# Performance work log

Measured on AMD Instinct MI355X. Metric: run time of the kernel, lower is better.

Reference implementation:

```python
import jax, jax.numpy as jnp
import numpy as np

LN_EPS = 1e-3  # keras LayerNormalization default
HEADS_GAT = 4

def _gelu(x):
    return jax.nn.gelu(x, approximate=False)  # keras 'gelu' is exact

def _ln(x, g, b):
    m = jnp.mean(x, axis=-1, keepdims=True)
    v = jnp.var(x, axis=-1, keepdims=True)
    return (x - m) / jnp.sqrt(v + LN_EPS) * g + b

def _gat(x, mask, w, a_src, a_dst, bias, heads):
    # dense-masked GAT: attention restricted to adj > 0.5 (self-loops present
    # since cosine-sim diagonal is 1). x: [BS, N, F]
    BS, N, _ = x.shape
    D = w.shape[1] // heads
    h = (x @ w).reshape(BS, N, heads, D)
    es = jnp.einsum('bnhd,hd->bnh', h, a_src)  # source term
    ed = jnp.einsum('bnhd,hd->bnh', h, a_dst)  # destination term
    # e[b,i,j,h]: edge j -> i
    e = jax.nn.leaky_relu(ed[:, :, None, :] + es[:, None, :, :], 0.2)
    e = jnp.where(mask[None, :, :, None], e, -1e9)
    alpha = jax.nn.softmax(e, axis=2)  # softmax over sources j
    out = jnp.einsum('bijh,bjhd->bihd', alpha, h).reshape(BS, N, heads * D)
    return out + bias

def _mha(x, wq, bq, wk, bk, wv, bv, wo, bo):
    q = jnp.einsum('bsf,fhd->bshd', x, wq) + bq
    k = jnp.einsum('bsf,fhd->bshd', x, wk) + bk
    v = jnp.einsum('bsf,fhd->bshd', x, wv) + bv
    s = jnp.einsum('bshd,bthd->bhst', q, k) / jnp.sqrt(jnp.asarray(q.shape[-1], x.dtype))
    a = jax.nn.softmax(s, axis=-1)
    o = jnp.einsum('bhst,bthd->bshd', a, v)
    return jnp.einsum('bshd,hdf->bsf', o, wo) + bo

def setup_inputs() -> dict:
    key = jax.random.key(0)
    ks = jax.random.split(key, 40)
    B, S, N = 4, 16, 400
    HID, OUT, DM, MH, DK, FF = 16, 32, 32, 2, 16, 64
    f32 = jnp.float32
    def glorot(k, shape, fin, fout):
        return jax.random.normal(k, shape, f32) * np.sqrt(2.0 / (fin + fout)).astype(np.float32)
    return {
        'x': jax.random.normal(ks[0], (B, S, N, 3), f32),
        'adj_embed': glorot(ks[1], (N, HID), N, HID),
        'proj_w': glorot(ks[2], (3, HID), 3, HID), 'proj_b': jnp.zeros((HID,), f32),
        'g1_w': glorot(ks[3], (HID, HID), HID, HID),
        'g1_asrc': glorot(ks[4], (4, HID // 4), HID, 4), 'g1_adst': glorot(ks[5], (4, HID // 4), HID, 4),
        'g1_b': jnp.zeros((HID,), f32),
        'g2_w': glorot(ks[6], (HID, OUT), HID, OUT),
        'g2_asrc': glorot(ks[7], (4, OUT // 4), OUT, 4), 'g2_adst': glorot(ks[8], (4, OUT // 4), OUT, 4),
        'g2_b': jnp.zeros((OUT,), f32),
        'wq': glorot(ks[9], (DM, MH, DK), DM, DM), 'bq': jnp.zeros((MH, DK), f32),
        'wk': glorot(ks[10], (DM, MH, DK), DM, DM), 'bk': jnp.zeros((MH, DK), f32),
        'wv': glorot(ks[11], (DM, MH, DK), DM, DM), 'bv': jnp.zeros((MH, DK), f32),
        'wo': glorot(ks[12], (MH, DK, DM), DM, DM), 'bo': jnp.zeros((DM,), f32),
        'ln1_g': jnp.ones((DM,), f32), 'ln1_b': jnp.zeros((DM,), f32),
        'f_w1': glorot(ks[13], (DM, FF), DM, FF), 'f_b1': jnp.zeros((FF,), f32),
        'f_w2': glorot(ks[14], (FF, DM), FF, DM), 'f_b2': jnp.zeros((DM,), f32),
        'ln2_g': jnp.ones((DM,), f32), 'ln2_b': jnp.zeros((DM,), f32),
        'r_w1': glorot(ks[15], (DM, 16), DM, 16), 'r_b1': jnp.zeros((16,), f32),
        'r_w2': glorot(ks[16], (16, 1), 16, 1), 'r_b2': jnp.zeros((1,), f32),
    }

def reference(x, adj_embed, proj_w, proj_b, g1_w, g1_asrc, g1_adst, g1_b,
              g2_w, g2_asrc, g2_adst, g2_b, wq, bq, wk, bk, wv, bv, wo, bo,
              ln1_g, ln1_b, f_w1, f_b1, f_w2, f_b2, ln2_g, ln2_b,
              r_w1, r_b1, r_w2, r_b2):
    B, S, N, _ = x.shape
    DM = 32
    xs = x.reshape(B * S, N, 3)
    # adaptive adjacency: cosine similarity of learned node embeddings
    emb = adj_embed / jnp.sqrt(jnp.maximum(jnp.sum(adj_embed * adj_embed, -1, keepdims=True), 1e-12))
    mask = (emb @ emb.T) > 0.5  # [N, N], shared across batch
    h = xs @ proj_w + proj_b
    h = _gelu(_gat(h, mask, g1_w, g1_asrc, g1_adst, g1_b, HEADS_GAT))
    h = _gat(h, mask, g2_w, g2_asrc, g2_adst, g2_b, HEADS_GAT)  # [B*S, N, 32]
    # faithful to source: plain reshape (no transpose) into temporal batch
    t = h.reshape(B, S, N, DM).reshape(B * N, S, DM)
    attn = _mha(t, wq, bq, wk, bk, wv, bv, wo, bo)
    t = _ln(t + attn, ln1_g, ln1_b)
    f = _gelu(t @ f_w1 + f_b1) @ f_w2 + f_b2
    t = _ln(t + f, ln2_g, ln2_b)
    t = t.reshape(B, N, S, DM)
    m = jnp.mean(t, axis=2)  # [B, N, 32]
    r = _gelu(m @ r_w1 + r_b1) @ r_w2 + r_b2
    return r[..., 0]  # [B, N]
```

## Files before the change

kernel.cpp:

```cpp
#include <hip/hip_runtime.h>

#define DEVINL __device__ __forceinline__

DEVINL float gelu_exact(float x){ return 0.5f * x * (1.0f + erff(x * 0.70710678118654752f)); }
DEVINL float lrelu02(float x){ return x >= 0.0f ? x : 0.2f * x; }

#define NN    400
#define NROWS 25600
#define NSEQ  1600

#define OFF_NBR  0u
#define OFF_CNT  320000u
#define OFF_HP1  321600u
#define OFF_ES1  1960000u
#define OFF_ED1  2369600u
#define OFF_HP2  2779200u
#define OFF_ES2  6056000u
#define OFF_ED2  6465600u
#define OFF_H2   6875200u

__global__ __launch_bounds__(256) void k_nbr_pre1(const float* __restrict__ emb,
    const float* __restrict__ x, const float* __restrict__ pw, const float* __restrict__ pb,
    const float* __restrict__ g1w, const float* __restrict__ as1, const float* __restrict__ ad1,
    unsigned short* __restrict__ nlist, int* __restrict__ cnt,
    float* __restrict__ hp1, float* __restrict__ es1, float* __restrict__ ed1){
  if (blockIdx.x < NN){
    const int i = blockIdx.x;
    const int lane = threadIdx.x;
    if (lane >= 64) return;
    double ai[16];
    double si = 0.0;
    #pragma unroll
    for (int k = 0; k < 16; k++){ ai[k] = (double)emb[i*16 + k]; si += ai[k]*ai[k]; }
    const double rni = 1.0 / sqrt(fmax(si, 1e-12));
    int base = 0;
    #pragma unroll
    for (int t = 0; t < 7; t++){
      const int j = t*64 + lane;
      bool valid = false;
      if (j < NN){
        double sj = 0.0, dp = 0.0;
        #pragma unroll
        for (int k = 0; k < 16; k++){
          double bv = (double)emb[j*16 + k];
          sj += bv*bv; dp += ai[k]*bv;
        }
        double c = dp * rni / sqrt(fmax(sj, 1e-12));
        valid = (c > 0.5);
      }
      unsigned long long bal = __ballot(valid);
      int pre = __popcll(bal & ((1ull << lane) - 1ull));
      if (valid) nlist[i*NN + base + pre] = (unsigned short)j;
      base += (int)__popcll(bal);
    }
    if (lane == 0) cnt[i] = base;
    return;
  }
  __shared__ float s_pw[48], s_pb[16], s_w[256], s_as[16], s_ad[16];
  const int tid = threadIdx.x;
  if (tid < 48) s_pw[tid] = pw[tid];
  if (tid < 16){ s_pb[tid] = pb[tid]; s_as[tid] = as1[tid]; s_ad[tid] = ad1[tid]; }
  s_w[tid] = g1w[tid];
  __syncthreads();
  const int row = (blockIdx.x - NN) * 256 + tid;
  if (row >= NROWS) return;
  float x0 = x[row*3+0], x1v = x[row*3+1], x2 = x[row*3+2];
  float h0[16];
  #pragma unroll
  for (int c = 0; c < 16; c++)
    h0[c] = s_pb[c] + x0 * s_pw[c] + x1v * s_pw[16+c] + x2 * s_pw[32+c];
  float hp[16];
  #pragma unroll
  for (int c = 0; c < 16; c++){
    float a = 0.f;
    #pragma unroll
    for (int k = 0; k < 16; k++) a += h0[k] * s_w[k*16 + c];
    hp[c] = a;
  }
  float4* hout = (float4*)(hp1 + (size_t)row * 16);
  hout[0] = make_float4(hp[0],hp[1],hp[2],hp[3]);
  hout[1] = make_float4(hp[4],hp[5],hp[6],hp[7]);
  hout[2] = make_float4(hp[8],hp[9],hp[10],hp[11]);
  hout[3] = make_float4(hp[12],hp[13],hp[14],hp[15]);
  #pragma unroll
  for (int h = 0; h < 4; h++){
    float es = 0.f, ed = 0.f;
    #pragma unroll
    for (int d = 0; d < 4; d++){ es += hp[h*4+d]*s_as[h*4+d]; ed += hp[h*4+d]*s_ad[h*4+d]; }
    es1[row*4 + h] = es;
    ed1[row*4 + h] = ed;
  }
}

__global__ __launch_bounds__(256) void k_gat1pre2(
    const float* __restrict__ hp1, const float* __restrict__ es1, const float* __restrict__ ed1,
    const unsigned short* __restrict__ nlist, const int* __restrict__ cnt,
    const float* __restrict__ g1b, const float* __restrict__ g2w,
    const float* __restrict__ as2, const float* __restrict__ ad2,
    float* __restrict__ hp2, float* __restrict__ es2, float* __restrict__ ed2){
  __shared__ float s_w[512], s_b1[16], s_as[32], s_ad[32];
  const int tid = threadIdx.x;
  s_w[tid] = g2w[tid]; s_w[tid+256] = g2w[tid+256];
  if (tid < 16) s_b1[tid] = g1b[tid];
  if (tid < 32){ s_as[tid] = as2[tid]; s_ad[tid] = ad2[tid]; }
  __syncthreads();
  const int row = blockIdx.x * 256 + tid;
  if (row >= NROWS) return;
  const int gb = row / NN;
  const int i  = row - gb * NN;
  const int n  = cnt[i];
  const unsigned short* nl = nlist + i * NN;
  const float4* esb = (const float4*)(es1 + (size_t)gb * NN * 4);
  const float*  hpb = hp1 + (size_t)gb * NN * 16;
  const float4 edv = *(const float4*)(ed1 + (size_t)row * 4);
  const float edr[4] = {edv.x, edv.y, edv.z, edv.w};
  float mx[4] = {-1e30f,-1e30f,-1e30f,-1e30f};
  for (int k0 = 0; k0 < n; k0 += 8){
    int jj[8]; float wv[8];
    #pragma unroll
    for (int u = 0; u < 8; u++){
      int kk = k0+u; jj[u] = (int)nl[kk < n ? kk : n-1]; wv[u] = (kk < n) ? 1.f : 0.f;
    }
    #pragma unroll
    for (int u = 0; u < 8; u++){
      float4 e4 = esb[jj[u]];
      mx[0] = fmaxf(mx[0], wv[u] > 0.5f ? e4.x : -1e30f);
      mx[1] = fmaxf(mx[1], wv[u] > 0.5f ? e4.y : -1e30f);
      mx[2] = fmaxf(mx[2], wv[u] > 0.5f ? e4.z : -1e30f);
      mx[3] = fmaxf(mx[3], wv[u] > 0.5f ? e4.w : -1e30f);
    }
  }
  float m[4];
  #pragma unroll
  for (int h = 0; h < 4; h++) m[h] = lrelu02(edr[h] + mx[h]);
  float den[4] = {0.f,0.f,0.f,0.f};
  float acc[16];
  #pragma unroll
  for (int d = 0; d < 16; d++) acc[d] = 0.f;
  for (int k0 = 0; k0 < n; k0 += 8){
    int jj[8]; float wv[8];
    #pragma unroll
    for (int u = 0; u < 8; u++){
      int kk = k0+u; jj[u] = (int)nl[kk < n ? kk : n-1]; wv[u] = (kk < n) ? 1.f : 0.f;
    }
    #pragma unroll
    for (int u = 0; u < 8; u++){
      float4 e4 = esb[jj[u]];
      const float4* hv = (const float4*)(hpb + (size_t)jj[u] * 16);
      float4 h0 = hv[0], h1 = hv[1], h2v = hv[2], h3 = hv[3];
      float p0 = wv[u] * __expf(lrelu02(edr[0]+e4.x) - m[0]); den[0] += p0;
      float p1 = wv[u] * __expf(lrelu02(edr[1]+e4.y) - m[1]); den[1] += p1;
      float p2 = wv[u] * __expf(lrelu02(edr[2]+e4.z) - m[2]); den[2] += p2;
      float p3 = wv[u] * __expf(lrelu02(edr[3]+e4.w) - m[3]); den[3] += p3;
      acc[0]  += p0*h0.x;  acc[1]  += p0*h0.y;  acc[2]  += p0*h0.z;  acc[3]  += p0*h0.w;
      acc[4]  += p1*h1.x;  acc[5]  += p1*h1.y;  acc[6]  += p1*h1.z;  acc[7]  += p1*h1.w;
      acc[8]  += p2*h2v.x; acc[9]  += p2*h2v.y; acc[10] += p2*h2v.z; acc[11] += p2*h2v.w;
      acc[12] += p3*h3.x;  acc[13] += p3*h3.y;  acc[14] += p3*h3.z;  acc[15] += p3*h3.w;
    }
  }
  float x1r[16];
  #pragma unroll
  for (int h = 0; h < 4; h++){
    float inv = 1.0f / den[h];
    #pragma unroll
    for (int d = 0; d < 4; d++)
      x1r[h*4+d] = gelu_exact(acc[h*4+d] * inv + s_b1[h*4+d]);
  }
  float hp[32];
  #pragma unroll
  for (int c = 0; c < 32; c++){
    float a = 0.f;
    #pragma unroll
    for (int k = 0; k < 16; k++) a += x1r[k] * s_w[k*32 + c];
    hp[c] = a;
  }
  float4* ho = (float4*)(hp2 + (size_t)row * 32);
  #pragma unroll
  for (int qd = 0; qd < 8; qd++)
    ho[qd] = make_float4(hp[qd*4], hp[qd*4+1], hp[qd*4+2], hp[qd*4+3]);
  #pragma unroll
  for (int h = 0; h < 4; h++){
    float es = 0.f, ed = 0.f;
    #pragma unroll
    for (int d = 0; d < 8; d++){ es += hp[h*8+d]*s_as[h*8+d]; ed += hp[h*8+d]*s_ad[h*8+d]; }
    es2[row*4 + h] = es;
    ed2[row*4 + h] = ed;
  }
}

__global__ __launch_bounds__(256) void k_gat2s(const float* __restrict__ hp,
    const float* __restrict__ es, const float* __restrict__ ed,
    const unsigned short* __restrict__ nlist, const int* __restrict__ cnt,
    const float* __restrict__ bias, float* __restrict__ outp){
  int idx = blockIdx.x * 256 + threadIdx.x;
  if (idx >= NROWS * 4) return;
  const int row = idx >> 2, h = idx & 3;
  const int b = row / NN;
  const int i = row - b * NN;
  const int n = cnt[i];
  const unsigned short* nl = nlist + i * NN;
  const float* esb = es + (size_t)b * NN * 4;
  const float* hpb = hp + (size_t)b * NN * 32;
  const float edh = ed[(size_t)row * 4 + h];
  float mx = -1e30f;
  for (int k0 = 0; k0 < n; k0 += 8){
    int jj[8]; float wv[8];
    #pragma unroll
    for (int u = 0; u < 8; u++){
      int kk = k0+u; jj[u] = (int)nl[kk < n ? kk : n-1]; wv[u] = (kk < n) ? 1.f : 0.f;
    }
    #pragma unroll
    for (int u = 0; u < 8; u++){
      float v = esb[jj[u]*4 + h];
      mx = fmaxf(mx, wv[u] > 0.5f ? v : -1e30f);
    }
  }
  const float m = lrelu02(edh + mx);
  float den = 0.f;
  float acc[8];
  #pragma unroll
  for (int d = 0; d < 8; d++) acc[d] = 0.f;
  for (int k0 = 0; k0 < n; k0 += 8){
    int jj[8]; float wv[8], ev[8];
    #pragma unroll
    for (int u = 0; u < 8; u++){
      int kk = k0+u; jj[u] = (int)nl[kk < n ? kk : n-1]; wv[u] = (kk < n) ? 1.f : 0.f;
    }
    #pragma unroll
    for (int u = 0; u < 8; u++) ev[u] = esb[jj[u]*4 + h];
    #pragma unroll
    for (int u = 0; u < 8; u++){
      float pv = wv[u] * __expf(lrelu02(edh + ev[u]) - m);
      den += pv;
      const float4* vp = (const float4*)(hpb + (size_t)jj[u]*32 + h*8);
      float4 v0 = vp[0], v1 = vp[1];
      acc[0] += pv*v0.x; acc[1] += pv*v0.y; acc[2] += pv*v0.z; acc[3] += pv*v0.w;
      acc[4] += pv*v1.x; acc[5] += pv*v1.y; acc[6] += pv*v1.z; acc[7] += pv*v1.w;
    }
  }
  const float invd = 1.0f / den;
  float* op = outp + (size_t)row * 32 + h * 8;
  #pragma unroll
  for (int d = 0; d < 8; d++) op[d] = acc[d] * invd + bias[h*8 + d];
}

struct TW { const float* p[20]; };

__global__ __launch_bounds__(256) void k_trans3(const float* __restrict__ h2, TW tw,
                                                float* __restrict__ out){
  __shared__ float Wq[1024], Wk[1024], Wv[1024], Wo[1024];
  __shared__ float Fw1[2048], Fw2[2048], Rw1[512];
  __shared__ float Bq[32], Bk[32], Bv[32], Bo[32], L1g[32], L1b[32];
  __shared__ float Fb1[64], Fb2[32], L2g[32], L2b[32], Rb1v[16], Rw2[16];
  __shared__ float Rb2s[1];
  __shared__ float SCR[4][2640];
  const int tid = threadIdx.x;
  const int w = tid >> 6, lane = tid & 63;
  for (int i = tid; i < 1024; i += 256){
    Wq[i] = tw.p[0][i]; Wk[i] = tw.p[2][i]; Wv[i] = tw.p[4][i]; Wo[i] = tw.p[6][i];
  }
  for (int i = tid; i < 2048; i += 256){ Fw1[i] = tw.p[10][i]; Fw2[i] = tw.p[12][i]; }
  for (int i = tid; i < 512; i += 256) Rw1[i] = tw.p[16][i];
  if (tid < 32){
    Bq[tid] = tw.p[1][tid]; Bk[tid] = tw.p[3][tid]; Bv[tid] = tw.p[5][tid]; Bo[tid] = tw.p[7][tid];
    L1g[tid] = tw.p[8][tid]; L1b[tid] = tw.p[9][tid]; Fb2[tid] = tw.p[13][tid];
    L2g[tid] = tw.p[14][tid]; L2b[tid] = tw.p[15][tid];
  }
  if (tid < 64) Fb1[tid] = tw.p[11][tid];
  if (tid < 16){ Rb1v[tid] = tw.p[17][tid]; Rw2[tid] = tw.p[18][tid]; }
  if (tid == 0) Rb2s[0] = tw.p[19][0];
  __syncthreads();

  float* Tw = SCR[w];
  float* Kw = Tw + 528;
  float* Vw = Tw + 1056;
  float* Sw = Tw + 1584;
  const int p = blockIdx.x * 4 + w;
  const int s = lane >> 2, cg = lane & 3, ob = cg * 8;

  {
    const float4* src = (const float4*)(h2 + (size_t)(p * 16 + s) * 32 + ob);
    float4 a0 = src[0], a1 = src[1];
    float* tr = Tw + s*33 + ob;
    tr[0]=a0.x; tr[1]=a0.y; tr[2]=a0.z; tr[3]=a0.w;
    tr[4]=a1.x; tr[5]=a1.y; tr[6]=a1.z; tr[7]=a1.w;
  }
  float q[8], kk[8], vv[8];
  #pragma unroll
  for (int u = 0; u < 8; u++){ q[u] = Bq[ob+u]; kk[u] = Bk[ob+u]; vv[u] = Bv[ob+u]; }
  for (int f = 0; f < 32; f++){
    float tv = Tw[s*33 + f];
    #pragma unroll
    for (int u = 0; u < 8; u++){
      q[u]  += tv * Wq[f*32 + ob + u];
      kk[u] += tv * Wk[f*32 + ob + u];
      vv[u] += tv * Wv[f*32 + ob + u];
    }
  }
  #pragma unroll
  for (int u = 0; u < 8; u++){
    Sw[s*33 + ob + u] = q[u];
    Kw[s*33 + ob + u] = kk[u];
    Vw[s*33 + ob + u] = vv[u];
  }
  const int ai = (lane >> 1) & 15;
  const int hb = (lane >> 5) * 16 + (lane & 1) * 8;
  float qreg[8];
  #pragma unroll
  for (int u = 0; u < 8; u++) qreg[u] = Sw[ai*33 + hb + u];
  float sc[16];
  float mx = -1e30f;
  #pragma unroll
  for (int j = 0; j < 16; j++){
    float d = 0.f;
    #pragma unroll
    for (int u = 0; u < 8; u++) d += qreg[u] * Kw[j*33 + hb + u];
    d += __shfl_xor(d, 1);
    d *= 0.25f;
    sc[j] = d;
    mx = fmaxf(mx, d);
  }
  float den = 0.f;
  #pragma unroll
  for (int j = 0; j < 16; j++){ sc[j] = __expf(sc[j] - mx); den += sc[j]; }
  const float ainv = 1.0f / den;
  float at[8];
  #pragma unroll
  for (int u = 0; u < 8; u++) at[u] = 0.f;
  #pragma unroll
  for (int j = 0; j < 16; j++){
    float al = sc[j];
    #pragma unroll
    for (int u = 0; u < 8; u++) at[u] += al * Vw[j*33 + hb + u];
  }
  #pragma unroll
  for (int u = 0; u < 8; u++) Sw[ai*33 + hb + u] = at[u] * ainv;
  float xr[8];
  #pragma unroll
  for (int u = 0; u < 8; u++) xr[u] = Bo[ob + u];
  for (int i2 = 0; i2 < 32; i2++){
    float av = Sw[s*33 + i2];
    #pragma unroll
    for (int u = 0; u < 8; u++) xr[u] += av * Wo[i2*32 + ob + u];
  }
  #pragma unroll
  for (int u = 0; u < 8; u++) xr[u] += Tw[s*33 + ob + u];
  float sm = 0.f, sq = 0.f;
  #pragma unroll
  for (int u = 0; u < 8; u++){ sm += xr[u]; sq += xr[u]*xr[u]; }
  sm += __shfl_xor(sm, 1); sq += __shfl_xor(sq, 1);
  sm += __shfl_xor(sm, 2); sq += __shfl_xor(sq, 2);
  {
    float mean = sm * (1.f/32.f);
    float var  = sq * (1.f/32.f) - mean*mean;
    float rinv = 1.0f / sqrtf(var + 1e-3f);
    #pragma unroll
    for (int u = 0; u < 8; u++)
      Tw[s*33 + ob + u] = (xr[u] - mean) * rinv * L1g[ob+u] + L1b[ob+u];
  }
  {
    const int cb = cg * 16;
    #pragma unroll
    for (int t = 0; t < 16; t++){
      int c = cb + t;
      float a = Fb1[c];
      for (int f = 0; f < 32; f++) a += Tw[s*33 + f] * Fw1[f*64 + c];
      Sw[s*66 + c] = gelu_exact(a);
    }
  }
  float y[8];
  #pragma unroll
  for (int u = 0; u < 8; u++) y[u] = Fb2[ob + u];
  for (int c = 0; c < 64; c++){
    float fv = Sw[s*66 + c];
    #pragma unroll
    for (int u = 0; u < 8; u++) y[u] += fv * Fw2[c*32 + ob + u];
  }
  #pragma unroll
  for (int u = 0; u < 8; u++) y[u] += Tw[s*33 + ob + u];
  sm = 0.f; sq = 0.f;
  #pragma unroll
  for (int u = 0; u < 8; u++){ sm += y[u]; sq += y[u]*y[u]; }
  sm += __shfl_xor(sm, 1); sq += __shfl_xor(sq, 1);
  sm += __shfl_xor(sm, 2); sq += __shfl_xor(sq, 2);
  float mean2 = sm * (1.f/32.f);
  float var2  = sq * (1.f/32.f) - mean2*mean2;
  float rinv2 = 1.0f / sqrtf(var2 + 1e-3f);
  float mv[8];
  #pragma unroll
  for (int u = 0; u < 8; u++){
    float v = (y[u] - mean2) * rinv2 * L2g[ob+u] + L2b[ob+u];
    v += __shfl_xor(v, 4);  v += __shfl_xor(v, 8);
    v += __shfl_xor(v, 16); v += __shfl_xor(v, 32);
    mv[u] = v * (1.f/16.f);
  }
  if (s == 0){
    #pragma unroll
    for (int u = 0; u < 8; u++) Tw[ob + u] = mv[u];
  }
  const int t = lane & 15;
  float hid = Rb1v[t];
  for (int o2 = 0; o2 < 32; o2++) hid += Tw[o2] * Rw1[o2*16 + t];
  hid = gelu_exact(hid) * Rw2[t];
  hid += __shfl_xor(hid, 1); hid += __shfl_xor(hid, 2);
  hid += __shfl_xor(hid, 4); hid += __shfl_xor(hid, 8);
  if (lane == 0) out[p] = hid + Rb2s[0];
}

extern "C" void kernel_launch(void* const* d_in, const int* in_sizes, int n_in,
                              void* d_out, int out_size, void* d_ws, size_t ws_size,
                              hipStream_t stream){
  const float* x    = (const float*)d_in[0];
  const float* adj  = (const float*)d_in[1];
  const float* pw   = (const float*)d_in[2];
  const float* pb   = (const float*)d_in[3];
  const float* g1w  = (const float*)d_in[4];
  const float* g1as = (const float*)d_in[5];
  const float* g1ad = (const float*)d_in[6];
  const float* g1b  = (const float*)d_in[7];
  const float* g2w  = (const float*)d_in[8];
  const float* g2as = (const float*)d_in[9];
  const float* g2ad = (const float*)d_in[10];
  const float* g2b  = (const float*)d_in[11];

  char* ws = (char*)d_ws;
  unsigned short* nlist = (unsigned short*)(ws + OFF_NBR);
  int*   cnt = (int*)(ws + OFF_CNT);
  float* hp1 = (float*)(ws + OFF_HP1);
  float* es1 = (float*)(ws + OFF_ES1);
  float* ed1 = (float*)(ws + OFF_ED1);
  float* hp2 = (float*)(ws + OFF_HP2);
  float* es2 = (float*)(ws + OFF_ES2);
  float* ed2 = (float*)(ws + OFF_ED2);
  float* h2  = (float*)(ws + OFF_H2);

  TW tw;
  for (int t = 0; t < 20; t++) tw.p[t] = (const float*)d_in[12 + t];

  hipLaunchKernelGGL(k_nbr_pre1, dim3(NN + 100), dim3(256), 0, stream,
                     adj, x, pw, pb, g1w, g1as, g1ad, nlist, cnt, hp1, es1, ed1);
  hipLaunchKernelGGL(k_gat1pre2, dim3(100), dim3(256), 0, stream,
                     hp1, es1, ed1, nlist, cnt, g1b, g2w, g2as, g2ad, hp2, es2, ed2);
  hipLaunchKernelGGL(k_gat2s, dim3(400), dim3(256), 0, stream,
                     hp2, es2, ed2, nlist, cnt, g2b, h2);
  hipLaunchKernelGGL(k_trans3, dim3(NSEQ/4), dim3(256), 0, stream,
                     h2, tw, (float*)d_out);
}
```

Measured before the change: 71.02 us.

## Fuse second GAT aggregation into transformer kernel, dropping h2 round-trip

The separate second-layer GAT aggregation kernel is removed, and its per-row, per-head softmax-weighted neighbor gather now runs at the start of the transformer kernel. Each lane writes its result straight into the shared-memory tile instead of reading it from a global h2 buffer. This saves one launch and one global write and read of the layer output. In exchange the transformer kernel gets only 400 blocks and carries a heavy shared-memory footprint, so the gather-bound GAT work runs at lower occupancy and latency hiding may suffer.

```diff
diff --git a/kernel.cpp b/kernel.cpp
--- a/kernel.cpp
+++ b/kernel.cpp
@@ -17,7 +17,6 @@
 #define OFF_HP2  2779200u
 #define OFF_ES2  6056000u
 #define OFF_ED2  6465600u
-#define OFF_H2   6875200u
 
 __global__ __launch_bounds__(256) void k_nbr_pre1(const float* __restrict__ emb,
     const float* __restrict__ x, const float* __restrict__ pw, const float* __restrict__ pb,
@@ -188,70 +187,18 @@
   }
 }
 
-__global__ __launch_bounds__(256) void k_gat2s(const float* __restrict__ hp,
-    const float* __restrict__ es, const float* __restrict__ ed,
-    const unsigned short* __restrict__ nlist, const int* __restrict__ cnt,
-    const float* __restrict__ bias, float* __restrict__ outp){
-  int idx = blockIdx.x * 256 + threadIdx.x;
-  if (idx >= NROWS * 4) return;
-  const int row = idx >> 2, h = idx & 3;
-  const int b = row / NN;
-  const int i = row - b * NN;
-  const int n = cnt[i];
-  const unsigned short* nl = nlist + i * NN;
-  const float* esb = es + (size_t)b * NN * 4;
-  const float* hpb = hp + (size_t)b * NN * 32;
-  const float edh = ed[(size_t)row * 4 + h];
-  float mx = -1e30f;
-  for (int k0 = 0; k0 < n; k0 += 8){
-    int jj[8]; float wv[8];
-    #pragma unroll
-    for (int u = 0; u < 8; u++){
-      int kk = k0+u; jj[u] = (int)nl[kk < n ? kk : n-1]; wv[u] = (kk < n) ? 1.f : 0.f;
-    }
-    #pragma unroll
-    for (int u = 0; u < 8; u++){
-      float v = esb[jj[u]*4 + h];
-      mx = fmaxf(mx, wv[u] > 0.5f ? v : -1e30f);
-    }
-  }
-  const float m = lrelu02(edh + mx);
-  float den = 0.f;
-  float acc[8];
-  #pragma unroll
-  for (int d = 0; d < 8; d++) acc[d] = 0.f;
-  for (int k0 = 0; k0 < n; k0 += 8){
-    int jj[8]; float wv[8], ev[8];
-    #pragma unroll
-    for (int u = 0; u < 8; u++){
-      int kk = k0+u; jj[u] = (int)nl[kk < n ? kk : n-1]; wv[u] = (kk < n) ? 1.f : 0.f;
-    }
-    #pragma unroll
-    for (int u = 0; u < 8; u++) ev[u] = esb[jj[u]*4 + h];
-    #pragma unroll
-    for (int u = 0; u < 8; u++){
-      float pv = wv[u] * __expf(lrelu02(edh + ev[u]) - m);
-      den += pv;
-      const float4* vp = (const float4*)(hpb + (size_t)jj[u]*32 + h*8);
-      float4 v0 = vp[0], v1 = vp[1];
-      acc[0] += pv*v0.x; acc[1] += pv*v0.y; acc[2] += pv*v0.z; acc[3] += pv*v0.w;
-      acc[4] += pv*v1.x; acc[5] += pv*v1.y; acc[6] += pv*v1.z; acc[7] += pv*v1.w;
-    }
-  }
-  const float invd = 1.0f / den;
-  float* op = outp + (size_t)row * 32 + h * 8;
-  #pragma unroll
-  for (int d = 0; d < 8; d++) op[d] = acc[d] * invd + bias[h*8 + d];
-}
-
 struct TW { const float* p[20]; };
 
-__global__ __launch_bounds__(256) void k_trans3(const float* __restrict__ h2, TW tw,
-                                                float* __restrict__ out){
+__global__ __launch_bounds__(256) void k_trans7(
+    const float* __restrict__ hp2, const float* __restrict__ es2,
+    const float* __restrict__ ed2, const unsigned short* __restrict__ nlist,
+    const int* __restrict__ cnt, const float* __restrict__ g2b,
+    TW tw, float* __restrict__ out){
   __shared__ float Wq[1024], Wk[1024], Wv[1024], Wo[1024];
   __shared__ float Fw1[2048], Fw2[2048], Rw1[512];
   __shared__ float Bq[32], Bk[32], Bv[32], Bo[32], L1g[32], L1b[32];
   __shared__ float Fb1[64], Fb2[32], L2g[32], L2b[32], Rb1v[16], Rw2[16];
+  __shared__ float Gb2[32];
   __shared__ float Rb2s[1];
   __shared__ float SCR[4][2640];
   const int tid = threadIdx.x;
@@ -265,6 +212,7 @@
     Bq[tid] = tw.p[1][tid]; Bk[tid] = tw.p[3][tid]; Bv[tid] = tw.p[5][tid]; Bo[tid] = tw.p[7][tid];
     L1g[tid] = tw.p[8][tid]; L1b[tid] = tw.p[9][tid]; Fb2[tid] = tw.p[13][tid];
     L2g[tid] = tw.p[14][tid]; L2b[tid] = tw.p[15][tid];
+    Gb2[tid] = g2b[tid];
   }
   if (tid < 64) Fb1[tid] = tw.p[11][tid];
   if (tid < 16){ Rb1v[tid] = tw.p[17][tid]; Rw2[tid] = tw.p[18][tid]; }
@@ -279,11 +227,53 @@
   const int s = lane >> 2, cg = lane & 3, ob = cg * 8;
 
   {
-    const float4* src = (const float4*)(h2 + (size_t)(p * 16 + s) * 32 + ob);
-    float4 a0 = src[0], a1 = src[1];
+    const int r  = p * 16 + s;
+    const int gb = r / NN;
+    const int i  = r - gb * NN;
+    const int n  = cnt[i];
+    const unsigned short* nl = nlist + i * NN;
+    const int rbase = gb * NN;
+    const float edh = ed2[(size_t)r * 4 + cg];
+    float mx = -1e30f;
+    for (int k0 = 0; k0 < n; k0 += 8){
+      int jj[8]; float wv[8];
+      #pragma unroll
+      for (int u = 0; u < 8; u++){
+        int kk = k0+u; jj[u] = (int)nl[kk < n ? kk : n-1]; wv[u] = (kk < n) ? 1.f : 0.f;
+      }
+      #pragma unroll
+      for (int u = 0; u < 8; u++){
+        float v = es2[(size_t)(rbase + jj[u]) * 4 + cg];
+        mx = fmaxf(mx, wv[u] > 0.5f ? v : -1e30f);
+      }
+    }
+    const float m = lrelu02(edh + mx);
+    float den = 0.f;
+    float acc[8];
+    #pragma unroll
+    for (int d = 0; d < 8; d++) acc[d] = 0.f;
+    for (int k0 = 0; k0 < n; k0 += 8){
+      int jj[8]; float wv[8], ev[8];
+      #pragma unroll
+      for (int u = 0; u < 8; u++){
+        int kk = k0+u; jj[u] = (int)nl[kk < n ? kk : n-1]; wv[u] = (kk < n) ? 1.f : 0.f;
+      }
+      #pragma unroll
+      for (int u = 0; u < 8; u++) ev[u] = es2[(size_t)(rbase + jj[u]) * 4 + cg];
+      #pragma unroll
+      for (int u = 0; u < 8; u++){
+        float pv = wv[u] * __expf(lrelu02(edh + ev[u]) - m);
+        den += pv;
+        const float4* vp = (const float4*)(hp2 + (size_t)(rbase + jj[u]) * 32 + cg * 8);
+        float4 v0 = vp[0], v1 = vp[1];
+        acc[0] += pv*v0.x; acc[1] += pv*v0.y; acc[2] += pv*v0.z; acc[3] += pv*v0.w;
+        acc[4] += pv*v1.x; acc[5] += pv*v1.y; acc[6] += pv*v1.z; acc[7] += pv*v1.w;
+      }
+    }
+    const float invd = 1.0f / den;
     float* tr = Tw + s*33 + ob;
-    tr[0]=a0.x; tr[1]=a0.y; tr[2]=a0.z; tr[3]=a0.w;
-    tr[4]=a1.x; tr[5]=a1.y; tr[6]=a1.z; tr[7]=a1.w;
+    #pragma unroll
+    for (int u = 0; u < 8; u++) tr[u] = acc[u] * invd + Gb2[ob + u];
   }
   float q[8], kk[8], vv[8];
   #pragma unroll
@@ -432,7 +422,6 @@
   float* hp2 = (float*)(ws + OFF_HP2);
   float* es2 = (float*)(ws + OFF_ES2);
   float* ed2 = (float*)(ws + OFF_ED2);
-  float* h2  = (float*)(ws + OFF_H2);
 
   TW tw;
   for (int t = 0; t < 20; t++) tw.p[t] = (const float*)d_in[12 + t];
@@ -441,8 +430,6 @@
                      adj, x, pw, pb, g1w, g1as, g1ad, nlist, cnt, hp1, es1, ed1);
   hipLaunchKernelGGL(k_gat1pre2, dim3(100), dim3(256), 0, stream,
                      hp1, es1, ed1, nlist, cnt, g1b, g2w, g2as, g2ad, hp2, es2, ed2);
-  hipLaunchKernelGGL(k_gat2s, dim3(400), dim3(256), 0, stream,
-                     hp2, es2, ed2, nlist, cnt, g2b, h2);
-  hipLaunchKernelGGL(k_trans3, dim3(NSEQ/4), dim3(256), 0, stream,
-                     h2, tw, (float*)d_out);
+  hipLaunchKernelGGL(k_trans7, dim3(NSEQ/4), dim3(256), 0, stream,
+                     hp2, es2, ed2, nlist, cnt, g2b, tw, (float*)d_out);
 }
```

After: 64.86 us (median of 2 runs). -8.7%, faster.
